# Performance work log

Measured on AMD Instinct MI355X. Metric: run time of the kernel, lower is better.

Reference implementation:

```python
import jax, jax.numpy as jnp
import numpy as np

N_NODES = 50000
D_MODEL = 128
N_EDGES = 600000
HIDDEN = 128
EDGE_FEAT = 2 * D_MODEL + 2  # 258


def setup_inputs() -> dict:
    key = jax.random.key(0)
    k = jax.random.split(key, 8)
    H = jax.random.normal(k[0], (N_NODES, D_MODEL), dtype=jnp.float32)
    edge_index = jax.random.randint(k[1], (2, N_EDGES), 0, N_NODES, dtype=jnp.int64)
    S_e = jax.random.uniform(k[2], (N_EDGES,), dtype=jnp.float32)
    F_e = jax.random.uniform(k[3], (N_EDGES,), dtype=jnp.float32)
    W1 = jax.random.normal(k[4], (EDGE_FEAT, HIDDEN), dtype=jnp.float32) * (1.0 / np.sqrt(EDGE_FEAT))
    b1 = jnp.zeros((HIDDEN,), dtype=jnp.float32)
    W2 = jax.random.normal(k[5], (HIDDEN, 1), dtype=jnp.float32) * (1.0 / np.sqrt(HIDDEN))
    b2 = jnp.zeros((1,), dtype=jnp.float32)
    return {"H": H, "edge_index": edge_index, "S_e": S_e, "F_e": F_e,
            "W1": W1, "b1": b1, "W2": W2, "b2": b2}


def reference(H, edge_index, S_e, F_e, W1, b1, W2, b2):
    # Gather endpoint node features: [E, D]
    H_u = H[edge_index[0]]
    H_v = H[edge_index[1]]
    H_diff = jnp.abs(H_u - H_v)
    H_prod = H_u * H_v
    # [E, 2D+2]
    edge_features = jnp.concatenate(
        [H_diff, H_prod, S_e[:, None], F_e[:, None]], axis=1)
    # 2-layer MLP with SiLU (dropout is identity in eval mode)
    h = jax.nn.silu(edge_features @ W1 + b1)
    a_e = (h @ W2 + b2)[:, 0]  # [E]
    return a_e
```

## Files before the change

kernel.cpp:

```cpp
#include <hip/hip_runtime.h>


typedef _Float16       half8   __attribute__((ext_vector_type(8)));
typedef _Float16       half4v  __attribute__((ext_vector_type(4)));
typedef unsigned short ushort8 __attribute__((ext_vector_type(8)));
typedef float          f32x4   __attribute__((ext_vector_type(4)));

#define NSEG       8
#define W1T_STRIDE 288

__device__ __forceinline__ float silu_f(float x) {
    return x / (1.0f + __expf(-x));
}

__device__ __forceinline__ void canon(int u, int v, int& a, int& b) {
    const int sw = (u ^ v) & 1;
    a = sw ? v : u;
    b = sw ? u : v;
}


__global__ __launch_bounds__(256)
void cvt_hist_kernel(const float* __restrict__ H, _Float16* __restrict__ Hh,
                     int n4, const int* __restrict__ eidx,
                     int* __restrict__ hist, int E, int ASZ, int BBINS) {
    int i = blockIdx.x * blockDim.x + threadIdx.x;
    if (i < n4) {
        const float4 f = ((const float4*)H)[i];
        half4v h;
        h[0] = (_Float16)f.x; h[1] = (_Float16)f.y;
        h[2] = (_Float16)f.z; h[3] = (_Float16)f.w;
        ((half4v*)Hh)[i] = h;
    }
    if (i < E) {
        int a, b;
        canon(eidx[i], eidx[E + i], a, b);
        atomicAdd(&hist[(a / ASZ) * BBINS + (b >> 3)], 1);
    }
}

__global__ __launch_bounds__(256)
void scan_kernel(int* __restrict__ hist, int* __restrict__ bsum,
                 int NB, int nb1, int* __restrict__ flag,
                 int* __restrict__ vbs, int BBINS, int E) {
    __shared__ int s[256];
    __shared__ int lastBlk;
    const int t = threadIdx.x;
    const int i = blockIdx.x * 256 + t;
    const int v = (i < NB) ? hist[i] : 0;
    s[t] = v;
    __syncthreads();
    for (int off = 1; off < 256; off <<= 1) {
        const int x = (t >= off) ? s[t - off] : 0;
        __syncthreads();
        s[t] += x;
        __syncthreads();
    }
    if (i < NB) hist[i] = s[t] - v;
    if (t == 255) bsum[blockIdx.x] = s[255];
    __threadfence();
    if (t == 0) lastBlk = (atomicAdd(flag, 1) == (int)gridDim.x - 1);
    __syncthreads();
    if (!lastBlk) return;
    const int bv = (t < nb1) ? atomicAdd(&bsum[t], 0) : 0;
    s[t] = bv;
    __syncthreads();
    for (int off = 1; off < 256; off <<= 1) {
        const int x = (t >= off) ? s[t - off] : 0;
        __syncthreads();
        s[t] += x;
        __syncthreads();
    }
    if (t < nb1) bsum[t] = s[t] - bv;
    __syncthreads();
    if (t < NSEG) {
        const int idx = t * BBINS;
        vbs[t] = atomicAdd(&hist[idx], 0) + bsum[idx >> 8];
    } else if (t == NSEG) {
        vbs[NSEG] = E;
    }
}

__global__ __launch_bounds__(256)
void scatter_kernel(const int* __restrict__ eidx, const float* __restrict__ Se,
                    const float* __restrict__ Fe, int* __restrict__ ofs,
                    const int* __restrict__ bsum,
                    int4* __restrict__ recs, int E, int ASZ, int BBINS) {
    int e = blockIdx.x * blockDim.x + threadIdx.x;
    if (e < E) {
        int a, b;
        canon(eidx[e], eidx[E + e], a, b);
        const int key = (a / ASZ) * BBINS + (b >> 3);
        const int pos = atomicAdd(&ofs[key], 1) + bsum[key >> 8];
        _Float16 sh = (_Float16)Se[e];
        _Float16 fh = (_Float16)Fe[e];
        unsigned pk = (unsigned)*(unsigned short*)&sh
                    | ((unsigned)*(unsigned short*)&fh << 16);
        recs[pos] = make_int4(a, b, e, (int)pk);
    }
}


__device__ __forceinline__ void stage_w1(const float* __restrict__ W1,
                                         const float* __restrict__ b1,
                                         _Float16* __restrict__ w1t, int tid) {
    const int n = tid & 127;
    const int g = tid >> 7;
    #pragma unroll
    for (int i = 0; i < 5; ++i) {
        const int kb = g + (i << 3);
        if (kb < 32) {
            half8 tmp;
            #pragma unroll
            for (int j = 0; j < 8; ++j) {
                const int kp  = (kb << 3) + j;
                const int c   = kp >> 5;
                const int k32 = kp & 31;
                const int src = ((c & 1) << 7) + ((c >> 1) << 5) + k32;
                tmp[j] = (_Float16)W1[src * 128 + n];
            }
            *(half8*)&w1t[n * W1T_STRIDE + ((kb ^ (n & 7)) << 3)] = tmp;
        } else if (kb < 36) {
            const int k32b = (kb - 32) << 3;
            half8 tmp;
            #pragma unroll
            for (int j = 0; j < 8; ++j) {
                const int k32 = k32b + j;
                float v = 0.f;
                if (k32 == 0)      v = W1[32768 + n];
                else if (k32 == 1) v = W1[32896 + n];
                else if (k32 == 2) v = b1[n];
                tmp[j] = (_Float16)v;
            }
            *(half8*)&w1t[n * W1T_STRIDE + (kb << 3)] = tmp;
        }
    }
}


__device__ __forceinline__ void edge_tile16(
    const _Float16* __restrict__ Hh, const int4* __restrict__ recs,
    const _Float16* __restrict__ w1t,
    const f32x4* __restrict__ w2r, float b2v, float* __restrict__ out,
    int ebase, int elim, int q, int cb, int swz)
{
    const int e = min(ebase + cb, elim - 1);
    const int4 r = recs[e];
    const int a = r.x, b = r.y;
    const unsigned pk = (unsigned)r.w;
    const unsigned short sl = (unsigned short)(pk & 0xFFFF);
    const unsigned short fl = (unsigned short)(pk >> 16);

    const _Float16* up = Hh + (size_t)a * 128;
    const _Float16* vp = Hh + (size_t)b * 128;

    f32x4 acc[8];
    #pragma unroll
    for (int t = 0; t < 8; ++t) acc[t] = (f32x4){0.f, 0.f, 0.f, 0.f};

    #pragma unroll
    for (int c8 = 0; c8 < 4; ++c8) {
        const half8 u8 = *(const half8*)(up + (c8 << 5) + (q << 3));
        const half8 v8 = *(const half8*)(vp + (c8 << 5) + (q << 3));
        half8 d8 = u8 - v8;
        ushort8 du = *(ushort8*)&d8;
        du = du & (unsigned short)0x7FFF;
        const half8 ae = *(half8*)&du;
        const half8 ao = u8 * v8;

        const int kb0 = ((c8 << 3) + q) ^ swz;
        const int kb1 = ((c8 << 3) + 4 + q) ^ swz;
        #pragma unroll
        for (int t = 0; t < 8; ++t) {
            const half8 b0 = *(const half8*)&w1t[((t << 4) + cb) * W1T_STRIDE + (kb0 << 3)];
            acc[t] = __builtin_amdgcn_mfma_f32_16x16x32_f16(b0, ae, acc[t], 0, 0, 0);
        }
        #pragma unroll
        for (int t = 0; t < 8; ++t) {
            const half8 b1f = *(const half8*)&w1t[((t << 4) + cb) * W1T_STRIDE + (kb1 << 3)];
            acc[t] = __builtin_amdgcn_mfma_f32_16x16x32_f16(b1f, ao, acc[t], 0, 0, 0);
        }
    }

    half8 aE;
    #pragma unroll
    for (int j = 0; j < 8; ++j) aE[j] = (_Float16)0.f;
    if (q == 0) {
        aE[0] = *(const _Float16*)&sl;
        aE[1] = *(const _Float16*)&fl;
        aE[2] = (_Float16)1.0f;
    }
    #pragma unroll
    for (int t = 0; t < 8; ++t) {
        const half8 bE = *(const half8*)&w1t[((t << 4) + cb) * W1T_STRIDE + ((32 + q) << 3)];
        acc[t] = __builtin_amdgcn_mfma_f32_16x16x32_f16(bE, aE, acc[t], 0, 0, 0);
    }

    float rs = 0.f;
    #pragma unroll
    for (int t = 0; t < 8; ++t) {
        const f32x4 av = acc[t];
        const f32x4 wv = w2r[t];
        #pragma unroll
        for (int rr = 0; rr < 4; ++rr)
            rs += silu_f(av[rr]) * wv[rr];
    }
    rs += __shfl_xor(rs, 16);
    rs += __shfl_xor(rs, 32);

    if (q == 0 && ebase + cb < elim) out[r.z] = rs + b2v;
}


__global__ __launch_bounds__(1024, 2)
void edgegate_seg(const _Float16* __restrict__ Hh,
                  const int4*  __restrict__ recs,
                  const int*   __restrict__ vbs,
                  int*         __restrict__ ctr,
                  const float* __restrict__ W1,
                  const float* __restrict__ b1,
                  const float* __restrict__ W2,
                  const float* __restrict__ b2,
                  float*       __restrict__ out)
{
    __shared__ _Float16 w1t[128 * W1T_STRIDE];
    __shared__ int tkt[2];
    const int tid = threadIdx.x;
    stage_w1(W1, b1, w1t, tid);

    int xcd;
    asm volatile("s_getreg_b32 %0, hwreg(HW_REG_XCC_ID)" : "=s"(xcd));
    xcd &= (NSEG - 1);

    const int lane = tid & 63;
    const int wave = tid >> 6;
    const int q    = lane >> 4;
    const int cb   = lane & 15;
    const int swz  = cb & 7;
    const float b2v = b2[0];
    f32x4 w2r[8];
    #pragma unroll
    for (int t = 0; t < 8; ++t)
        w2r[t] = *(const f32x4*)&W2[(t << 4) + (q << 2)];

    int p = 0;
    for (int sidx = 0; sidx < NSEG; ++sidx) {
        const int seg = (xcd + sidx) & (NSEG - 1);
        const int vs  = vbs[seg];
        const int ve  = vbs[seg + 1];
        const int ner = ve - vs;
        if (ner <= 0) continue;
        const int Tt = (ner + 255) >> 8;

        __syncthreads();
        if (tid == 0) tkt[p] = atomicAdd(&ctr[seg], 1);
        __syncthreads();
        int t0 = tkt[p];
        while (t0 < Tt) {
            const int pn = p ^ 1;
            if (tid == 0) tkt[pn] = atomicAdd(&ctr[seg], 1);
            const int ebase = vs + (t0 << 8) + (wave << 4);
            edge_tile16(Hh, recs, w1t, w2r, b2v, out, ebase, ve, q, cb, swz);
            __syncthreads();
            p = pn;
            t0 = tkt[p];
        }
    }
}


__global__ __launch_bounds__(1024, 2)
void edgegate_fb(const float* __restrict__ H,
                 const _Float16* __restrict__ Hh,
                 const int*   __restrict__ eidx,
                 const float* __restrict__ Se,
                 const float* __restrict__ Fe,
                 const float* __restrict__ W1,
                 const float* __restrict__ b1,
                 const float* __restrict__ W2,
                 const float* __restrict__ b2,
                 float*       __restrict__ out,
                 int E, int ntiles, int useF16)
{
    __shared__ _Float16 w1t[128 * W1T_STRIDE];
    const int tid = threadIdx.x;
    stage_w1(W1, b1, w1t, tid);

    const int lane = tid & 63;
    const int wave = tid >> 6;
    const int q    = lane >> 4;
    const int cb   = lane & 15;
    const int swz  = cb & 7;
    const float b2v = b2[0];
    f32x4 w2r[8];
    #pragma unroll
    for (int t = 0; t < 8; ++t)
        w2r[t] = *(const f32x4*)&W2[(t << 4) + (q << 2)];

    __syncthreads();

    for (int tile = blockIdx.x; tile < ntiles; tile += gridDim.x) {
        const int ebase = tile * 256 + wave * 16;
        int e = ebase + cb;
        if (e >= E) e = E - 1;
        const int u = eidx[e];
        const int v = eidx[E + e];
        const float sfe = Se[e];
        const float ffe = Fe[e];

        f32x4 acc[8];
        #pragma unroll
        for (int t = 0; t < 8; ++t) acc[t] = (f32x4){0.f, 0.f, 0.f, 0.f};

        #pragma unroll
        for (int c8 = 0; c8 < 4; ++c8) {
            half8 ae, ao;
            if (useF16) {
                const _Float16* up = Hh + (size_t)u * 128;
                const _Float16* vp = Hh + (size_t)v * 128;
                const half8 u8 = *(const half8*)(up + (c8 << 5) + (q << 3));
                const half8 v8 = *(const half8*)(vp + (c8 << 5) + (q << 3));
                half8 d8 = u8 - v8;
                ushort8 du = *(ushort8*)&d8;
                du = du & (unsigned short)0x7FFF;
                ae = *(half8*)&du;
                ao = u8 * v8;
            } else {
                const float* up = H + (size_t)u * 128;
                const float* vp = H + (size_t)v * 128;
                #pragma unroll
                for (int j = 0; j < 8; ++j) {
                    const float uu = up[(c8 << 5) + (q << 3) + j];
                    const float vv = vp[(c8 << 5) + (q << 3) + j];
                    ae[j] = (_Float16)fabsf(uu - vv);
                    ao[j] = (_Float16)(uu * vv);
                }
            }
            const int kb0 = ((c8 << 3) + q) ^ swz;
            const int kb1 = ((c8 << 3) + 4 + q) ^ swz;
            #pragma unroll
            for (int t = 0; t < 8; ++t) {
                const half8 b0 = *(const half8*)&w1t[((t << 4) + cb) * W1T_STRIDE + (kb0 << 3)];
                acc[t] = __builtin_amdgcn_mfma_f32_16x16x32_f16(b0, ae, acc[t], 0, 0, 0);
            }
            #pragma unroll
            for (int t = 0; t < 8; ++t) {
                const half8 b1f = *(const half8*)&w1t[((t << 4) + cb) * W1T_STRIDE + (kb1 << 3)];
                acc[t] = __builtin_amdgcn_mfma_f32_16x16x32_f16(b1f, ao, acc[t], 0, 0, 0);
            }
        }

        half8 aE;
        #pragma unroll
        for (int j = 0; j < 8; ++j) aE[j] = (_Float16)0.f;
        if (q == 0) {
            aE[0] = (_Float16)sfe;
            aE[1] = (_Float16)ffe;
            aE[2] = (_Float16)1.0f;
        }
        #pragma unroll
        for (int t = 0; t < 8; ++t) {
            const half8 bE = *(const half8*)&w1t[((t << 4) + cb) * W1T_STRIDE + ((32 + q) << 3)];
            acc[t] = __builtin_amdgcn_mfma_f32_16x16x32_f16(bE, aE, acc[t], 0, 0, 0);
        }

        float rs = 0.f;
        #pragma unroll
        for (int t = 0; t < 8; ++t) {
            const f32x4 av = acc[t];
            const f32x4 wv = w2r[t];
            #pragma unroll
            for (int rr = 0; rr < 4; ++rr)
                rs += silu_f(av[rr]) * wv[rr];
        }
        rs += __shfl_xor(rs, 16);
        rs += __shfl_xor(rs, 32);

        if (q == 0 && ebase + cb < E) out[ebase + cb] = rs + b2v;
    }
}


static inline size_t align256(size_t x) { return (x + 255) & ~(size_t)255; }

extern "C" void kernel_launch(void* const* d_in, const int* in_sizes, int n_in,
                              void* d_out, int out_size, void* d_ws, size_t ws_size,
                              hipStream_t stream)
{
    const float* H    = (const float*)d_in[0];
    const int*   eidx = (const int*)  d_in[1];
    const float* Se   = (const float*)d_in[2];
    const float* Fe   = (const float*)d_in[3];
    const float* W1   = (const float*)d_in[4];
    const float* b1   = (const float*)d_in[5];
    const float* W2   = (const float*)d_in[6];
    const float* b2   = (const float*)d_in[7];
    float* out = (float*)d_out;

    const int nH     = in_sizes[0];
    const int nNodes = nH / 128;
    const int E      = in_sizes[2];
    const int n4     = nH / 4;
    const int ntiles = (E + 255) / 256;

    const int ASZ   = (nNodes + NSEG - 1) / NSEG;
    const int BBINS = (nNodes + 7) >> 3;
    const int NB    = NSEG * BBINS;
    const int nb1   = (NB + 255) / 256;

    const size_t hhB    = (size_t)nH * sizeof(_Float16);
    const size_t off_g  = align256(hhB);
    const size_t off_bs = align256(off_g + (size_t)(NB + 16) * 4);
    const size_t off_vb = align256(off_bs + 256 * 4);
    const size_t off_r  = align256(off_vb + 16 * 4);
    const size_t need   = off_r + (size_t)E * sizeof(int4);

    if (ws_size >= need && nb1 <= 256) {
        _Float16* Hh   = (_Float16*)((char*)d_ws);
        int*      hist = (int*)     ((char*)d_ws + off_g);
        int*      ctr  = hist + NB;
        int*      flag = hist + NB + 8;
        int*      bsum = (int*)     ((char*)d_ws + off_bs);
        int*      vbs  = (int*)     ((char*)d_ws + off_vb);
        int4*     recs = (int4*)    ((char*)d_ws + off_r);

        const int ncvh = (n4 > E) ? n4 : E;
        hipMemsetAsync(hist, 0, (size_t)(NB + 16) * sizeof(int), stream);
        hipLaunchKernelGGL(cvt_hist_kernel, dim3((ncvh + 255) / 256), dim3(256),
                           0, stream, H, Hh, n4, eidx, hist, E, ASZ, BBINS);
        hipLaunchKernelGGL(scan_kernel, dim3(nb1), dim3(256), 0, stream,
                           hist, bsum, NB, nb1, flag, vbs, BBINS, E);
        hipLaunchKernelGGL(scatter_kernel, dim3((E + 255) / 256), dim3(256),
                           0, stream, eidx, Se, Fe, hist, bsum, recs,
                           E, ASZ, BBINS);
        hipLaunchKernelGGL(edgegate_seg, dim3(512), dim3(1024), 0, stream,
                           Hh, recs, vbs, ctr, W1, b1, W2, b2, out);
    } else if (ws_size >= hhB) {
        _Float16* Hh = (_Float16*)d_ws;
        const int grid = (512 < ntiles) ? 512 : ntiles;
        hipLaunchKernelGGL(cvt_hist_kernel, dim3((n4 + 255) / 256), dim3(256),
                           0, stream, H, Hh, n4, eidx, (int*)nullptr, 0, 1, 1);
        hipLaunchKernelGGL(edgegate_fb, dim3(grid), dim3(1024), 0, stream,
                           H, Hh, eidx, Se, Fe, W1, b1, W2, b2, out, E, ntiles, 1);
    } else {
        const int grid = (512 < ntiles) ? 512 : ntiles;
        hipLaunchKernelGGL(edgegate_fb, dim3(grid), dim3(1024), 0, stream,
                           H, (const _Float16*)nullptr, eidx, Se, Fe, W1, b1, W2, b2,
                           out, E, ntiles, 0);
    }
}
```

Baseline: 294.3 us.

## Process two 16-edge groups per wave to reuse W1 LDS fragments

Each wave now handles 32 edges per tile, issuing two MFMAs per W1 fragment read from shared memory, which halves the LDS traffic per edge. Blocks shrink from 1024 to 512 threads so that a 256-edge tile is still covered, and the W1 staging loop is adjusted for the smaller thread count. The fallback path switches to 128-edge tiles. In exchange, doubling the accumulators raises register pressure and may reduce the number of resident waves.

```diff
diff --git a/kernel.cpp b/kernel.cpp
--- a/kernel.cpp
+++ b/kernel.cpp
@@ -107,10 +107,10 @@
     const int n = tid & 127;
     const int g = tid >> 7;
     #pragma unroll
-    for (int i = 0; i < 5; ++i) {
-        const int kb = g + (i << 3);
+    for (int i = 0; i < 9; ++i) {
+        const int kb = g + (i << 2);
+        half8 tmp;
         if (kb < 32) {
-            half8 tmp;
             #pragma unroll
             for (int j = 0; j < 8; ++j) {
                 const int kp  = (kb << 3) + j;
@@ -120,9 +120,8 @@
                 tmp[j] = (_Float16)W1[src * 128 + n];
             }
             *(half8*)&w1t[n * W1T_STRIDE + ((kb ^ (n & 7)) << 3)] = tmp;
-        } else if (kb < 36) {
+        } else {
             const int k32b = (kb - 32) << 3;
-            half8 tmp;
             #pragma unroll
             for (int j = 0; j < 8; ++j) {
                 const int k32 = k32b + j;
@@ -138,81 +137,107 @@
 }
 
 
-__device__ __forceinline__ void edge_tile16(
+__device__ __forceinline__ void edge_tile32(
     const _Float16* __restrict__ Hh, const int4* __restrict__ recs,
     const _Float16* __restrict__ w1t,
     const f32x4* __restrict__ w2r, float b2v, float* __restrict__ out,
     int ebase, int elim, int q, int cb, int swz)
 {
-    const int e = min(ebase + cb, elim - 1);
-    const int4 r = recs[e];
-    const int a = r.x, b = r.y;
-    const unsigned pk = (unsigned)r.w;
-    const unsigned short sl = (unsigned short)(pk & 0xFFFF);
-    const unsigned short fl = (unsigned short)(pk >> 16);
-
-    const _Float16* up = Hh + (size_t)a * 128;
-    const _Float16* vp = Hh + (size_t)b * 128;
-
-    f32x4 acc[8];
-    #pragma unroll
-    for (int t = 0; t < 8; ++t) acc[t] = (f32x4){0.f, 0.f, 0.f, 0.f};
+    const int eA = min(ebase + cb, elim - 1);
+    const int eB = min(ebase + 16 + cb, elim - 1);
+    const int4 rA = recs[eA];
+    const int4 rB = recs[eB];
+
+    const _Float16* upA = Hh + (size_t)rA.x * 128;
+    const _Float16* vpA = Hh + (size_t)rA.y * 128;
+    const _Float16* upB = Hh + (size_t)rB.x * 128;
+    const _Float16* vpB = Hh + (size_t)rB.y * 128;
+
+    f32x4 accA[8], accB[8];
+    #pragma unroll
+    for (int t = 0; t < 8; ++t) {
+        accA[t] = (f32x4){0.f, 0.f, 0.f, 0.f};
+        accB[t] = (f32x4){0.f, 0.f, 0.f, 0.f};
+    }
 
     #pragma unroll
     for (int c8 = 0; c8 < 4; ++c8) {
-        const half8 u8 = *(const half8*)(up + (c8 << 5) + (q << 3));
-        const half8 v8 = *(const half8*)(vp + (c8 << 5) + (q << 3));
-        half8 d8 = u8 - v8;
-        ushort8 du = *(ushort8*)&d8;
-        du = du & (unsigned short)0x7FFF;
-        const half8 ae = *(half8*)&du;
-        const half8 ao = u8 * v8;
+        const half8 u8A = *(const half8*)(upA + (c8 << 5) + (q << 3));
+        const half8 v8A = *(const half8*)(vpA + (c8 << 5) + (q << 3));
+        const half8 u8B = *(const half8*)(upB + (c8 << 5) + (q << 3));
+        const half8 v8B = *(const half8*)(vpB + (c8 << 5) + (q << 3));
+        half8 dA = u8A - v8A;
+        half8 dB = u8B - v8B;
+        ushort8 duA = *(ushort8*)&dA; duA = duA & (unsigned short)0x7FFF;
+        ushort8 duB = *(ushort8*)&dB; duB = duB & (unsigned short)0x7FFF;
+        const half8 aeA = *(half8*)&duA;
+        const half8 aeB = *(half8*)&duB;
+        const half8 aoA = u8A * v8A;
+        const half8 aoB = u8B * v8B;
 
         const int kb0 = ((c8 << 3) + q) ^ swz;
         const int kb1 = ((c8 << 3) + 4 + q) ^ swz;
         #pragma unroll
         for (int t = 0; t < 8; ++t) {
             const half8 b0 = *(const half8*)&w1t[((t << 4) + cb) * W1T_STRIDE + (kb0 << 3)];
-            acc[t] = __builtin_amdgcn_mfma_f32_16x16x32_f16(b0, ae, acc[t], 0, 0, 0);
+            accA[t] = __builtin_amdgcn_mfma_f32_16x16x32_f16(b0, aeA, accA[t], 0, 0, 0);
+            accB[t] = __builtin_amdgcn_mfma_f32_16x16x32_f16(b0, aeB, accB[t], 0, 0, 0);
         }
         #pragma unroll
         for (int t = 0; t < 8; ++t) {
             const half8 b1f = *(const half8*)&w1t[((t << 4) + cb) * W1T_STRIDE + (kb1 << 3)];
-            acc[t] = __builtin_amdgcn_mfma_f32_16x16x32_f16(b1f, ao, acc[t], 0, 0, 0);
-        }
-    }
-
-    half8 aE;
-    #pragma unroll
-    for (int j = 0; j < 8; ++j) aE[j] = (_Float16)0.f;
+            accA[t] = __builtin_amdgcn_mfma_f32_16x16x32_f16(b1f, aoA, accA[t], 0, 0, 0);
+            accB[t] = __builtin_amdgcn_mfma_f32_16x16x32_f16(b1f, aoB, accB[t], 0, 0, 0);
+        }
+    }
+
+    half8 aEA, aEB;
+    #pragma unroll
+    for (int j = 0; j < 8; ++j) { aEA[j] = (_Float16)0.f; aEB[j] = (_Float16)0.f; }
     if (q == 0) {
-        aE[0] = *(const _Float16*)&sl;
-        aE[1] = *(const _Float16*)&fl;
-        aE[2] = (_Float16)1.0f;
+        const unsigned short slA = (unsigned short)((unsigned)rA.w & 0xFFFF);
+        const unsigned short flA = (unsigned short)((unsigned)rA.w >> 16);
+        const unsigned short slB = (unsigned short)((unsigned)rB.w & 0xFFFF);
+        const unsigned short flB = (unsigned short)((unsigned)rB.w >> 16);
+        aEA[0] = *(const _Float16*)&slA;
+        aEA[1] = *(const _Float16*)&flA;
+        aEA[2] = (_Float16)1.0f;
+        aEB[0] = *(const _Float16*)&slB;
+        aEB[1] = *(const _Float16*)&flB;
+        aEB[2] = (_Float16)1.0f;
     }
     #pragma unroll
     for (int t = 0; t < 8; ++t) {
         const half8 bE = *(const half8*)&w1t[((t << 4) + cb) * W1T_STRIDE + ((32 + q) << 3)];
-        acc[t] = __builtin_amdgcn_mfma_f32_16x16x32_f16(bE, aE, acc[t], 0, 0, 0);
-    }
-
-    float rs = 0.f;
+        accA[t] = __builtin_amdgcn_mfma_f32_16x16x32_f16(bE, aEA, accA[t], 0, 0, 0);
+        accB[t] = __builtin_amdgcn_mfma_f32_16x16x32_f16(bE, aEB, accB[t], 0, 0, 0);
+    }
+
+    float rsA = 0.f, rsB = 0.f;
     #pragma unroll
     for (int t = 0; t < 8; ++t) {
-        const f32x4 av = acc[t];
-        const f32x4 wv = w2r[t];
-        #pragma unroll
-        for (int rr = 0; rr < 4; ++rr)
-            rs += silu_f(av[rr]) * wv[rr];
-    }
-    rs += __shfl_xor(rs, 16);
-    rs += __shfl_xor(rs, 32);
-
-    if (q == 0 && ebase + cb < elim) out[r.z] = rs + b2v;
-}
-
-
-__global__ __launch_bounds__(1024, 2)
+        const f32x4 avA = accA[t];
+        const f32x4 avB = accB[t];
+        const f32x4 wv  = w2r[t];
+        #pragma unroll
+        for (int rr = 0; rr < 4; ++rr) {
+            rsA += silu_f(avA[rr]) * wv[rr];
+            rsB += silu_f(avB[rr]) * wv[rr];
+        }
+    }
+    rsA += __shfl_xor(rsA, 16);
+    rsA += __shfl_xor(rsA, 32);
+    rsB += __shfl_xor(rsB, 16);
+    rsB += __shfl_xor(rsB, 32);
+
+    if (q == 0) {
+        if (ebase + cb < elim)      out[rA.z] = rsA + b2v;
+        if (ebase + 16 + cb < elim) out[rB.z] = rsB + b2v;
+    }
+}
+
+
+__global__ __launch_bounds__(512, 2)
 void edgegate_seg(const _Float16* __restrict__ Hh,
                   const int4*  __restrict__ recs,
                   const int*   __restrict__ vbs,
@@ -259,8 +284,8 @@
         while (t0 < Tt) {
             const int pn = p ^ 1;
             if (tid == 0) tkt[pn] = atomicAdd(&ctr[seg], 1);
-            const int ebase = vs + (t0 << 8) + (wave << 4);
-            edge_tile16(Hh, recs, w1t, w2r, b2v, out, ebase, ve, q, cb, swz);
+            const int ebase = vs + (t0 << 8) + (wave << 5);
+            edge_tile32(Hh, recs, w1t, w2r, b2v, out, ebase, ve, q, cb, swz);
             __syncthreads();
             p = pn;
             t0 = tkt[p];
@@ -269,7 +294,7 @@
 }
 
 
-__global__ __launch_bounds__(1024, 2)
+__global__ __launch_bounds__(512, 2)
 void edgegate_fb(const float* __restrict__ H,
                  const _Float16* __restrict__ Hh,
                  const int*   __restrict__ eidx,
@@ -300,7 +325,7 @@
     __syncthreads();
 
     for (int tile = blockIdx.x; tile < ntiles; tile += gridDim.x) {
-        const int ebase = tile * 256 + wave * 16;
+        const int ebase = tile * 128 + wave * 16;
         int e = ebase + cb;
         if (e >= E) e = E - 1;
         const int u = eidx[e];
@@ -401,7 +426,7 @@
     const int nNodes = nH / 128;
     const int E      = in_sizes[2];
     const int n4     = nH / 4;
-    const int ntiles = (E + 255) / 256;
+    const int ntiles = (E + 127) / 128;
 
     const int ASZ   = (nNodes + NSEG - 1) / NSEG;
     const int BBINS = (nNodes + 7) >> 3;
@@ -433,18 +458,18 @@
         hipLaunchKernelGGL(scatter_kernel, dim3((E + 255) / 256), dim3(256),
                            0, stream, eidx, Se, Fe, hist, bsum, recs,
                            E, ASZ, BBINS);
-        hipLaunchKernelGGL(edgegate_seg, dim3(512), dim3(1024), 0, stream,
+        hipLaunchKernelGGL(edgegate_seg, dim3(512), dim3(512), 0, stream,
                            Hh, recs, vbs, ctr, W1, b1, W2, b2, out);
     } else if (ws_size >= hhB) {
         _Float16* Hh = (_Float16*)d_ws;
         const int grid = (512 < ntiles) ? 512 : ntiles;
         hipLaunchKernelGGL(cvt_hist_kernel, dim3((n4 + 255) / 256), dim3(256),
                            0, stream, H, Hh, n4, eidx, (int*)nullptr, 0, 1, 1);
-        hipLaunchKernelGGL(edgegate_fb, dim3(grid), dim3(1024), 0, stream,
+        hipLaunchKernelGGL(edgegate_fb, dim3(grid), dim3(512), 0, stream,
                            H, Hh, eidx, Se, Fe, W1, b1, W2, b2, out, E, ntiles, 1);
     } else {
         const int grid = (512 < ntiles) ? 512 : ntiles;
-        hipLaunchKernelGGL(edgegate_fb, dim3(grid), dim3(1024), 0, stream,
+        hipLaunchKernelGGL(edgegate_fb, dim3(grid), dim3(512), 0, stream,
                            H, (const _Float16*)nullptr, eidx, Se, Fe, W1, b1, W2, b2,
                            out, E, ntiles, 0);
     }
```

Result: no change. 299.3 us (+1.7%).
